# Kernel tuning notes

Hardware: AMD Instinct MI355X
Metric: run time of the kernel (lower is better)

The kernel has to match this reference:

```python
import jax, jax.numpy as jnp
import numpy as np

EPS = 1e-08

def _compute_W(V, C, eps=EPS):
    # W = H_k ... H_1, applied sequentially as in the torch loop
    W = jnp.eye(C, dtype=V.dtype)
    def step(W, v):
        v = v / (jnp.linalg.norm(v) + eps)
        # H @ W = W - 2 v (v^T W)
        W = W - 2.0 * jnp.outer(v, v @ W)
        return W, None
    W, _ = jax.lax.scan(step, W, V)
    return W

def setup_inputs() -> dict:
    key = jax.random.key(0)
    k1, k2 = jax.random.split(key)
    x = jax.random.normal(k1, (16, 512, 64, 64), dtype=jnp.float32)
    V = jax.random.normal(k2, (32, 512), dtype=jnp.float32)
    return {"x": x, "V": V}

def reference(x, V):
    B, C, H, Wd = x.shape
    W = _compute_W(V, C)  # [C, C] orthogonal
    # 1x1 conv: out[b,o,h,w] = sum_c W[o,c] * x[b,c,h,w]
    return jnp.einsum('oc,bchw->bohw', W, x)
```

## Files before the change

### kernel.cpp

```cpp
#include <hip/hip_runtime.h>
#include <hip/hip_bf16.h>
#include <stdint.h>
#include <stddef.h>

#define HH_EPS 1e-8f

typedef __attribute__((ext_vector_type(8))) short short8;
typedef __attribute__((ext_vector_type(4))) float f32x4;

#define CDIM 512
#define SDIM 4096
#define BM 256
#define BN 64
#define BK 32
#define NSTEP 16

__device__ __forceinline__ size_t wt_idx(int o, int c) {
    return (((size_t)(c >> 5) * 32 + (o >> 4)) * 64
            + (size_t)((c >> 3) & 3) * 16 + (o & 15)) * 8 + (c & 7);
}

__global__ void compute_w(const float* __restrict__ V,
                          __hip_bfloat16* __restrict__ Wt) {
    const int wave = threadIdx.x >> 6;
    const int lane = threadIdx.x & 63;
    const int jA = (blockIdx.x * 4 + wave) * 2;
    const int jB = jA + 1;
    const int ib = lane * 8;

    float wA[8], wB[8];
    #pragma unroll
    for (int r = 0; r < 8; r++) {
        wA[r] = (ib + r == jA) ? 1.0f : 0.0f;
        wB[r] = (ib + r == jB) ? 1.0f : 0.0f;
    }
    float4 c0 = *(const float4*)(V + ib);
    float4 c1 = *(const float4*)(V + ib + 4);

    for (int k = 0; k < 32; k++) {
        const float v[8] = {c0.x, c0.y, c0.z, c0.w, c1.x, c1.y, c1.z, c1.w};
        if (k < 31) {
            c0 = *(const float4*)(V + (size_t)(k + 1) * 512 + ib);
            c1 = *(const float4*)(V + (size_t)(k + 1) * 512 + ib + 4);
        }
        float dA = 0.0f, dB = 0.0f, ss = 0.0f;
        #pragma unroll
        for (int r = 0; r < 8; r++) {
            dA += v[r] * wA[r];
            dB += v[r] * wB[r];
            ss += v[r] * v[r];
        }
        #pragma unroll
        for (int off = 32; off > 0; off >>= 1) {
            dA += __shfl_xor(dA, off);
            dB += __shfl_xor(dB, off);
            ss += __shfl_xor(ss, off);
        }
        const float t = sqrtf(ss) + HH_EPS;
        const float scale = 2.0f / (t * t);
        const float tA = scale * dA, tB = scale * dB;
        #pragma unroll
        for (int r = 0; r < 8; r++) {
            wA[r] -= tA * v[r];
            wB[r] -= tB * v[r];
        }
    }
    #pragma unroll
    for (int r = 0; r < 8; r++) {
        Wt[wt_idx(ib + r, jA)] = __float2bfloat16(wA[r]);
        Wt[wt_idx(ib + r, jB)] = __float2bfloat16(wB[r]);
    }
}

__device__ __forceinline__ void gld_lds16(const void* g, void* l) {
    __builtin_amdgcn_global_load_lds(
        (const __attribute__((address_space(1))) uint32_t*)g,
        (__attribute__((address_space(3))) uint32_t*)l, 16, 0, 0);
}

template<int N> __device__ __forceinline__ void wait_vm() {
    __builtin_amdgcn_s_waitcnt((N & 15) | ((N >> 4) << 14) | (7 << 4) | (15 << 8));
}

__device__ __forceinline__ void lds_barrier() {
    __builtin_amdgcn_s_waitcnt(0xC07F);
    __builtin_amdgcn_s_barrier();
}

constexpr int vm_pre(int kt) { return (kt + 3 < NSTEP) ? 8 : 0; }

__global__ __launch_bounds__(256, 3) void hh_gemm(
    const float* __restrict__ x,
    const __hip_bfloat16* __restrict__ Wt,
    float* __restrict__ out)
{
    __shared__ __attribute__((aligned(16))) __hip_bfloat16 Albuf[2][BM * BK];
    __shared__ __attribute__((aligned(16))) __hip_bfloat16 Bbuf[2][BN * BK];

    const int tid  = threadIdx.x;
    const int wave = tid >> 6, lane = tid & 63;
    const int ow = wave;
    const int quad = lane >> 4, l16 = lane & 15;

    const int bid = blockIdx.x;
    const int op  = bid & 1;
    const int nt  = (bid >> 1) & 63;
    const int b   = bid >> 7;
    const int n0  = nt * BN;

    const float* xb = x + (size_t)b * CDIM * SDIM;
    const int bn = tid & 63;
    const int kq = wave;
    const float* xp0 = xb + (size_t)(kq * 8) * SDIM + n0 + bn;

    f32x4 acc[4][4];
    #pragma unroll
    for (int mi = 0; mi < 4; mi++)
        #pragma unroll
        for (int oi = 0; oi < 4; oi++) {
            f32x4 z = {0.0f, 0.0f, 0.0f, 0.0f};
            acc[mi][oi] = z;
        }

    float pfB[3][8];

    auto loadA = [&](int kt, int p) {
        const char* gbase = (const char*)Wt
            + ((size_t)kt * 32 + op * 16 + ow * 4) * 1024 + (size_t)lane * 16;
        char* lbase = (char*)&Albuf[p][0] + (size_t)(ow * 4) * 1024;
        #pragma unroll
        for (int i = 0; i < 4; i++)
            gld_lds16(gbase + (size_t)i * 1024, lbase + (size_t)i * 1024);
    };
    auto loadB = [&](int kt, float* dst) {
        const float* p = xp0 + (size_t)kt * BK * SDIM;
        #pragma unroll
        for (int j = 0; j < 8; j++) dst[j] = p[(size_t)j * SDIM];
    };
    auto writeB = [&](int buf, const float* src) {
        short8 pk;
        #pragma unroll
        for (int j = 0; j < 8; j++) {
            __hip_bfloat16 h = __float2bfloat16(src[j]);
            pk[j] = *(short*)&h;
        }
        *(short8*)(&Bbuf[buf][(size_t)(((bn >> 4) * 4 + kq) * 16 + (bn & 15)) * 8]) = pk;
    };

    loadA(0, 0);
    loadB(0, pfB[0]);
    loadB(1, pfB[1]);
    loadB(2, pfB[2]);
    writeB(0, pfB[0]);
    wait_vm<16>();
    lds_barrier();

#define DO_STEP(KT)                                                            \
    {                                                                          \
        constexpr int p = (KT) & 1;                                            \
        if constexpr ((KT) + 1 < NSTEP) loadA((KT) + 1, p ^ 1);                \
        if constexpr ((KT) + 3 < NSTEP) loadB((KT) + 3, pfB[(KT) % 3]);        \
        short8 afr[4], bfr[4];                                                 \
        _Pragma("unroll")                                                      \
        for (int mi = 0; mi < 4; mi++)                                         \
            afr[mi] = *(const short8*)(&Bbuf[p][(size_t)(mi * 64 + lane) * 8]);\
        _Pragma("unroll")                                                      \
        for (int oi = 0; oi < 4; oi++)                                         \
            bfr[oi] = *(const short8*)(&Albuf[p][(size_t)((ow * 4 + oi) * 64   \
                                                          + lane) * 8]);      \
        _Pragma("unroll")                                                      \
        for (int mi = 0; mi < 4; mi++)                                         \
            _Pragma("unroll")                                                  \
            for (int oi = 0; oi < 4; oi++)                                     \
                acc[mi][oi] = __builtin_amdgcn_mfma_f32_16x16x32_bf16(         \
                    afr[mi], bfr[oi], acc[mi][oi], 0, 0, 0);                   \
        if constexpr ((KT) + 1 < NSTEP) {                                      \
            writeB(p ^ 1, pfB[((KT) + 1) % 3]);                                \
            wait_vm<vm_pre(KT)>();  \
            lds_barrier();                                                     \
        }                                                                      \
    }

    DO_STEP(0)  DO_STEP(1)  DO_STEP(2)  DO_STEP(3)
    DO_STEP(4)  DO_STEP(5)  DO_STEP(6)  DO_STEP(7)
    DO_STEP(8)  DO_STEP(9)  DO_STEP(10) DO_STEP(11)
    DO_STEP(12) DO_STEP(13) DO_STEP(14) DO_STEP(15)
#undef DO_STEP

    float* ob = out + (size_t)b * CDIM * SDIM + n0;
    #pragma unroll
    for (int oi = 0; oi < 4; oi++) {
        const int o = op * 256 + ow * 64 + oi * 16 + l16;
        #pragma unroll
        for (int mi = 0; mi < 4; mi++) {
            *(f32x4*)(ob + (size_t)o * SDIM + mi * 16 + quad * 4) = acc[mi][oi];
        }
    }
}

extern "C" void kernel_launch(void* const* d_in, const int* in_sizes, int n_in,
                              void* d_out, int out_size, void* d_ws, size_t ws_size,
                              hipStream_t stream) {
    const float* x = (const float*)d_in[0];
    const float* V = (const float*)d_in[1];
    float* out = (float*)d_out;

    __hip_bfloat16* Wt = (__hip_bfloat16*)d_ws;

    compute_w<<<64, 256, 0, stream>>>(V, Wt);
    hh_gemm<<<2048, 256, 0, stream>>>(x, Wt, out);
}
```

Before: 280.1 us.

## Drop LDS staging; load x and W directly into registers per wave

The GEMM kernel no longer stages W and x tiles through shared memory with barriers. Each 512-thread block now covers all 512 output channels for a 64-pixel tile. Every wave loads its own x fragments straight into registers, converts them to bf16, and loads its W fragments directly from global memory with register double/triple buffering. This removes LDS traffic and block barriers and halves the number of x reads per tile, since op-splitting is gone. The cost is that all 8 waves redundantly load the same x fragments, and register pressure is much higher (pfA holds 96 floats).

```diff
diff --git a/kernel.cpp b/kernel.cpp
--- a/kernel.cpp
+++ b/kernel.cpp
@@ -10,7 +10,6 @@
 
 #define CDIM 512
 #define SDIM 4096
-#define BM 256
 #define BN 64
 #define BK 32
 #define NSTEP 16
@@ -72,46 +71,22 @@
     }
 }
 
-__device__ __forceinline__ void gld_lds16(const void* g, void* l) {
-    __builtin_amdgcn_global_load_lds(
-        (const __attribute__((address_space(1))) uint32_t*)g,
-        (__attribute__((address_space(3))) uint32_t*)l, 16, 0, 0);
-}
-
-template<int N> __device__ __forceinline__ void wait_vm() {
-    __builtin_amdgcn_s_waitcnt((N & 15) | ((N >> 4) << 14) | (7 << 4) | (15 << 8));
-}
-
-__device__ __forceinline__ void lds_barrier() {
-    __builtin_amdgcn_s_waitcnt(0xC07F);
-    __builtin_amdgcn_s_barrier();
-}
-
-constexpr int vm_pre(int kt) { return (kt + 3 < NSTEP) ? 8 : 0; }
-
-__global__ __launch_bounds__(256, 3) void hh_gemm(
+__global__ __launch_bounds__(512, 2) void hh_gemm(
     const float* __restrict__ x,
     const __hip_bfloat16* __restrict__ Wt,
     float* __restrict__ out)
 {
-    __shared__ __attribute__((aligned(16))) __hip_bfloat16 Albuf[2][BM * BK];
-    __shared__ __attribute__((aligned(16))) __hip_bfloat16 Bbuf[2][BN * BK];
-
     const int tid  = threadIdx.x;
     const int wave = tid >> 6, lane = tid & 63;
-    const int ow = wave;
     const int quad = lane >> 4, l16 = lane & 15;
 
     const int bid = blockIdx.x;
-    const int op  = bid & 1;
-    const int nt  = (bid >> 1) & 63;
-    const int b   = bid >> 7;
+    const int b   = bid >> 6;
+    const int nt  = bid & 63;
     const int n0  = nt * BN;
 
-    const float* xb = x + (size_t)b * CDIM * SDIM;
-    const int bn = tid & 63;
-    const int kq = wave;
-    const float* xp0 = xb + (size_t)(kq * 8) * SDIM + n0 + bn;
+    const float* xb = x + (size_t)b * CDIM * SDIM + n0 + l16;
+    const short8* wp = (const short8*)Wt + (size_t)wave * 4 * 64 + lane;
 
     f32x4 acc[4][4];
     #pragma unroll
@@ -122,79 +97,55 @@
             acc[mi][oi] = z;
         }
 
-    float pfB[3][8];
+    float  pfA[3][4][8];
+    short8 wb[2][4];
 
-    auto loadA = [&](int kt, int p) {
-        const char* gbase = (const char*)Wt
-            + ((size_t)kt * 32 + op * 16 + ow * 4) * 1024 + (size_t)lane * 16;
-        char* lbase = (char*)&Albuf[p][0] + (size_t)(ow * 4) * 1024;
+    auto loadA = [&](int kt, int s) {
+        const float* p = xb + (size_t)(kt * BK + quad * 8) * SDIM;
         #pragma unroll
-        for (int i = 0; i < 4; i++)
-            gld_lds16(gbase + (size_t)i * 1024, lbase + (size_t)i * 1024);
+        for (int mi = 0; mi < 4; mi++)
+            #pragma unroll
+            for (int e = 0; e < 8; e++)
+                pfA[s][mi][e] = p[(size_t)e * SDIM + mi * 16];
     };
-    auto loadB = [&](int kt, float* dst) {
-        const float* p = xp0 + (size_t)kt * BK * SDIM;
+    auto loadW = [&](int kt, int s) {
+        const short8* p = wp + (size_t)kt * 32 * 64;
         #pragma unroll
-        for (int j = 0; j < 8; j++) dst[j] = p[(size_t)j * SDIM];
-    };
-    auto writeB = [&](int buf, const float* src) {
-        short8 pk;
-        #pragma unroll
-        for (int j = 0; j < 8; j++) {
-            __hip_bfloat16 h = __float2bfloat16(src[j]);
-            pk[j] = *(short*)&h;
-        }
-        *(short8*)(&Bbuf[buf][(size_t)(((bn >> 4) * 4 + kq) * 16 + (bn & 15)) * 8]) = pk;
+        for (int oi = 0; oi < 4; oi++)
+            wb[s][oi] = p[oi * 64];
     };
 
     loadA(0, 0);
-    loadB(0, pfB[0]);
-    loadB(1, pfB[1]);
-    loadB(2, pfB[2]);
-    writeB(0, pfB[0]);
-    wait_vm<16>();
-    lds_barrier();
+    loadW(0, 0);
+    loadA(1, 1);
 
-#define DO_STEP(KT)                                                            \
-    {                                                                          \
-        constexpr int p = (KT) & 1;                                            \
-        if constexpr ((KT) + 1 < NSTEP) loadA((KT) + 1, p ^ 1);                \
-        if constexpr ((KT) + 3 < NSTEP) loadB((KT) + 3, pfB[(KT) % 3]);        \
-        short8 afr[4], bfr[4];                                                 \
-        _Pragma("unroll")                                                      \
-        for (int mi = 0; mi < 4; mi++)                                         \
-            afr[mi] = *(const short8*)(&Bbuf[p][(size_t)(mi * 64 + lane) * 8]);\
-        _Pragma("unroll")                                                      \
-        for (int oi = 0; oi < 4; oi++)                                         \
-            bfr[oi] = *(const short8*)(&Albuf[p][(size_t)((ow * 4 + oi) * 64   \
-                                                          + lane) * 8]);      \
-        _Pragma("unroll")                                                      \
-        for (int mi = 0; mi < 4; mi++)                                         \
-            _Pragma("unroll")                                                  \
-            for (int oi = 0; oi < 4; oi++)                                     \
-                acc[mi][oi] = __builtin_amdgcn_mfma_f32_16x16x32_bf16(         \
-                    afr[mi], bfr[oi], acc[mi][oi], 0, 0, 0);                   \
-        if constexpr ((KT) + 1 < NSTEP) {                                      \
-            writeB(p ^ 1, pfB[((KT) + 1) % 3]);                                \
-            wait_vm<vm_pre(KT)>();  \
-            lds_barrier();                                                     \
-        }                                                                      \
+    #pragma unroll
+    for (int kt = 0; kt < NSTEP; kt++) {
+        if (kt + 1 < NSTEP) loadW(kt + 1, (kt + 1) & 1);
+        if (kt + 2 < NSTEP) loadA(kt + 2, (kt + 2) % 3);
+        const int s = kt % 3, w = kt & 1;
+        #pragma unroll
+        for (int mi = 0; mi < 4; mi++) {
+            short8 afr;
+            #pragma unroll
+            for (int e = 0; e < 8; e++) {
+                __hip_bfloat16 h = __float2bfloat16(pfA[s][mi][e]);
+                afr[e] = *(const short*)&h;
+            }
+            #pragma unroll
+            for (int oi = 0; oi < 4; oi++)
+                acc[mi][oi] = __builtin_amdgcn_mfma_f32_16x16x32_bf16(
+                    afr, wb[w][oi], acc[mi][oi], 0, 0, 0);
+        }
     }
-
-    DO_STEP(0)  DO_STEP(1)  DO_STEP(2)  DO_STEP(3)
-    DO_STEP(4)  DO_STEP(5)  DO_STEP(6)  DO_STEP(7)
-    DO_STEP(8)  DO_STEP(9)  DO_STEP(10) DO_STEP(11)
-    DO_STEP(12) DO_STEP(13) DO_STEP(14) DO_STEP(15)
-#undef DO_STEP
 
     float* ob = out + (size_t)b * CDIM * SDIM + n0;
     #pragma unroll
     for (int oi = 0; oi < 4; oi++) {
-        const int o = op * 256 + ow * 64 + oi * 16 + l16;
+        const int o = wave * 64 + oi * 16 + l16;
         #pragma unroll
-        for (int mi = 0; mi < 4; mi++) {
+        for (int mi = 0; mi < 4; mi++)
             *(f32x4*)(ob + (size_t)o * SDIM + mi * 16 + quad * 4) = acc[mi][oi];
-        }
     }
 }
 
@@ -208,5 +159,5 @@
     __hip_bfloat16* Wt = (__hip_bfloat16*)d_ws;
 
     compute_w<<<64, 256, 0, stream>>>(V, Wt);
-    hh_gemm<<<2048, 256, 0, stream>>>(x, Wt, out);
+    hh_gemm<<<1024, 512, 0, stream>>>(x, Wt, out);
 }
```

Result: slower. 316.0 us (+12.8%).
